# Kernel tuning notes

Measured on AMD Instinct MI355X. Metric: run time of the kernel, lower is better.

## Reference

```python
import jax, jax.numpy as jnp
import numpy as np

N_NODES = 20000
N_EDGES = 640000
IN_DIM, HID_DIM, OUT_DIM = 128, 128, 64


def setup_inputs() -> dict:
    key = jax.random.key(0)
    k = jax.random.split(key, 6)
    x = jax.random.normal(k[0], (N_NODES, IN_DIM), dtype=jnp.float32)
    edge_index = jax.random.randint(k[1], (2, N_EDGES), 0, N_NODES, dtype=jnp.int64)
    W1 = jax.random.normal(k[2], (IN_DIM, HID_DIM), dtype=jnp.float32) * (1.0 / np.sqrt(IN_DIM))
    b1 = jnp.zeros((HID_DIM,), dtype=jnp.float32)
    W2 = jax.random.normal(k[3], (HID_DIM, OUT_DIM), dtype=jnp.float32) * (1.0 / np.sqrt(HID_DIM))
    b2 = jnp.zeros((OUT_DIM,), dtype=jnp.float32)
    return {"x": x, "edge_index": edge_index, "W1": W1, "b1": b1, "W2": W2, "b2": b2}


def _gcn_conv(h, W, b, src, dst, n_nodes):
    # h' = D^-1/2 (A + I) D^-1/2 (h W) + b   (PyG GCNConv with self-loops)
    h = h @ W                                              # [N, F_out]
    ones = jnp.ones((src.shape[0],), dtype=h.dtype)
    deg = jax.ops.segment_sum(ones, dst, num_segments=n_nodes) + 1.0  # +1 for self-loop
    dinv = jax.lax.rsqrt(deg)                              # [N]
    w = dinv[src] * dinv[dst]                              # per-edge norm [E]
    msg = h[src] * w[:, None]                              # gather + scale [E, F_out]
    agg = jax.ops.segment_sum(msg, dst, num_segments=n_nodes)  # scatter-add [N, F_out]
    # self-loop contribution: norm_ii = dinv[i]^2
    return agg + h * (dinv * dinv)[:, None] + b


def reference(x, edge_index, W1, b1, W2, b2):
    src, dst = edge_index[0], edge_index[1]
    n = x.shape[0]
    h = _gcn_conv(x, W1, b1, src, dst, n)
    h = jax.nn.relu(h)
    # dropout is identity in eval mode (training=False)
    out = _gcn_conv(h, W2, b2, src, dst, n)
    return out
```

## Files before the change

### kernel.cpp

```cpp
#include <hip/hip_runtime.h>


#define N_NODES 20000
#define N_EDGES 640000
#define IN_DIM 128
#define HID_DIM 128
#define OUT_DIM 64

#define STRIDE 80
#define SCAT_NB (N_EDGES / 256)
#define G1_NB 625
#define G1_TASKS (2 * (N_NODES / 16))
#define PRE_ITEMS (128 * 128 + 64 * 128 + N_NODES)
#define PRE_NB ((PRE_ITEMS + 255) / 256)

typedef _Float16 half8_t __attribute__((ext_vector_type(8)));
typedef float float4_t __attribute__((ext_vector_type(4)));

__global__ __launch_bounds__(256) void k_pre(const float* __restrict__ W1,
                                             const float* __restrict__ W2,
                                             _Float16* __restrict__ WT1,
                                             _Float16* __restrict__ WT2,
                                             int* __restrict__ cnt) {
    int i = blockIdx.x * 256 + threadIdx.x;
    if (i < 128 * 128) {
        int c = i >> 7, k = i & 127;
        WT1[i] = (_Float16)W1[k * 128 + c];
    } else if (i < 128 * 128 + 64 * 128) {
        int o = i - 128 * 128;
        int c = o >> 7, k = o & 127;
        WT2[o] = (_Float16)W2[k * 64 + c];
    } else {
        int n = i - (128 * 128 + 64 * 128);
        if (n < N_NODES) cnt[n] = 0;
    }
}

__global__ __launch_bounds__(256) void k_front(const int* __restrict__ src,
                                               const int* __restrict__ dst,
                                               int* __restrict__ cnt,
                                               unsigned short* __restrict__ esrc_pad,
                                               const _Float16* __restrict__ WT1,
                                               const float* __restrict__ x,
                                               _Float16* __restrict__ G) {
    const int b = blockIdx.x, tid = threadIdx.x;
    if (b < SCAT_NB) {
        const int e = b * 256 + tid;
        const int s = __builtin_nontemporal_load(&src[e]);
        const int d = __builtin_nontemporal_load(&dst[e]);
        unsigned int rank = atomicAdd((unsigned int*)&cnt[d], 1u);
        if (rank < STRIDE) esrc_pad[d * STRIDE + rank] = (unsigned short)s;
        return;
    }
    const int wave = tid >> 6;
    const int lane = tid & 63;
    const int task = (b - SCAT_NB) * 4 + wave;
    if (task >= G1_TASKS) return;
    const int strip = task >> 1;
    const int nh = task & 1;
    const int row0 = strip * 16;
    const int mrow = row0 + (lane & 15);
    const int kq = (lane >> 4) * 8;

    half8_t af[4];
#pragma unroll
    for (int kc = 0; kc < 4; ++kc) {
        const float* ap = x + (size_t)mrow * 128 + kc * 32 + kq;
        float4_t f0 = __builtin_nontemporal_load((const float4_t*)ap);
        float4_t f1 = __builtin_nontemporal_load((const float4_t*)(ap + 4));
        half8_t h;
        h[0] = (_Float16)f0[0]; h[1] = (_Float16)f0[1];
        h[2] = (_Float16)f0[2]; h[3] = (_Float16)f0[3];
        h[4] = (_Float16)f1[0]; h[5] = (_Float16)f1[1];
        h[6] = (_Float16)f1[2]; h[7] = (_Float16)f1[3];
        af[kc] = h;
    }
    float4_t acc[4];
#pragma unroll
    for (int nt = 0; nt < 4; ++nt) acc[nt] = (float4_t)(0.0f);
#pragma unroll
    for (int nt = 0; nt < 4; ++nt) {
        const _Float16* wp = WT1 + (size_t)((nh * 4 + nt) * 16 + (lane & 15)) * 128 + kq;
#pragma unroll
        for (int kc = 0; kc < 4; ++kc) {
            half8_t bf = *(const half8_t*)(wp + kc * 32);
            acc[nt] = __builtin_amdgcn_mfma_f32_16x16x32_f16(af[kc], bf, acc[nt], 0, 0, 0);
        }
    }
#pragma unroll
    for (int r = 0; r < 4; ++r) {
        int row = row0 + (lane >> 4) * 4 + r;
#pragma unroll
        for (int nt = 0; nt < 4; ++nt)
            G[(size_t)row * 128 + nh * 64 + nt * 16 + (lane & 15)] =
                (_Float16)acc[nt][r];
    }
}

__global__ __launch_bounds__(256) void k_mid(const int* __restrict__ cnt,
                                             const unsigned short* __restrict__ esrc_pad,
                                             const _Float16* __restrict__ G,
                                             const _Float16* __restrict__ WT2,
                                             const float* __restrict__ b1,
                                             _Float16* __restrict__ g2) {
    __shared__ _Float16 h1[16][136];
    const int tid = threadIdx.x;
    const int wave = tid >> 6;
    const int lane = tid & 63;
    const int row0 = blockIdx.x * 16;
    const int eidx = lane >> 4;
    const int fl = lane & 15;

    for (int r4 = 0; r4 < 4; ++r4) {
        const int rr = wave * 4 + r4;
        const int node = row0 + rr;
        const int end = cnt[node];
        const float dvd = rsqrtf((float)end + 1.0f);
        const int base = node * STRIDE;

        float acc[8];
#pragma unroll
        for (int p = 0; p < 8; ++p) acc[p] = 0.0f;
        if (eidx == 0) {
            half8_t sv = *(const half8_t*)(G + (size_t)node * 128 + fl * 8);
#pragma unroll
            for (int p = 0; p < 8; ++p) acc[p] = dvd * (float)sv[p];
        }
        int j = 0;
        for (; j + 7 < end; j += 8) {
            int s0 = (int)__builtin_nontemporal_load(&esrc_pad[base + j + eidx]);
            int s1 = (int)__builtin_nontemporal_load(&esrc_pad[base + j + 4 + eidx]);
            float dv0 = rsqrtf((float)cnt[s0] + 1.0f);
            float dv1 = rsqrtf((float)cnt[s1] + 1.0f);
            half8_t r0 = *(const half8_t*)(G + (size_t)s0 * 128 + fl * 8);
            half8_t r1 = *(const half8_t*)(G + (size_t)s1 * 128 + fl * 8);
#pragma unroll
            for (int p = 0; p < 8; ++p)
                acc[p] += dv0 * (float)r0[p] + dv1 * (float)r1[p];
        }
        for (; j + 3 < end; j += 4) {
            int s = (int)__builtin_nontemporal_load(&esrc_pad[base + j + eidx]);
            float dvs = rsqrtf((float)cnt[s] + 1.0f);
            half8_t r = *(const half8_t*)(G + (size_t)s * 128 + fl * 8);
#pragma unroll
            for (int p = 0; p < 8; ++p) acc[p] += dvs * (float)r[p];
        }
        if (j < end) {
            int idx = j + eidx;
            int s = (int)__builtin_nontemporal_load(
                &esrc_pad[base + ((idx < end) ? idx : (end - 1))]);
            float valid = (idx < end) ? 1.0f : 0.0f;
            float dvs = rsqrtf((float)cnt[s] + 1.0f);
            half8_t r = *(const half8_t*)(G + (size_t)s * 128 + fl * 8);
#pragma unroll
            for (int p = 0; p < 8; ++p) acc[p] += valid * dvs * (float)r[p];
        }
#pragma unroll
        for (int p = 0; p < 8; ++p) {
            acc[p] += __shfl_xor(acc[p], 16, 64);
            acc[p] += __shfl_xor(acc[p], 32, 64);
        }
        if (eidx == 0) {
            float4_t c0 = *(const float4_t*)(b1 + fl * 8);
            float4_t c1 = *(const float4_t*)(b1 + fl * 8 + 4);
            half8_t o;
            o[0] = (_Float16)fmaxf(acc[0] * dvd + c0[0], 0.0f);
            o[1] = (_Float16)fmaxf(acc[1] * dvd + c0[1], 0.0f);
            o[2] = (_Float16)fmaxf(acc[2] * dvd + c0[2], 0.0f);
            o[3] = (_Float16)fmaxf(acc[3] * dvd + c0[3], 0.0f);
            o[4] = (_Float16)fmaxf(acc[4] * dvd + c1[0], 0.0f);
            o[5] = (_Float16)fmaxf(acc[5] * dvd + c1[1], 0.0f);
            o[6] = (_Float16)fmaxf(acc[6] * dvd + c1[2], 0.0f);
            o[7] = (_Float16)fmaxf(acc[7] * dvd + c1[3], 0.0f);
            *(half8_t*)&h1[rr][fl * 8] = o;
        }
    }
    __syncthreads();

    const int fr = lane & 15;
    const int kq = (lane >> 4) * 8;
    half8_t af[4];
#pragma unroll
    for (int kc = 0; kc < 4; ++kc)
        af[kc] = *(const half8_t*)&h1[fr][kc * 32 + kq];
    float4_t acc2 = (float4_t)(0.0f);
    const _Float16* wp = WT2 + (size_t)(wave * 16 + fr) * 128 + kq;
#pragma unroll
    for (int kc = 0; kc < 4; ++kc) {
        half8_t bf = *(const half8_t*)(wp + kc * 32);
        acc2 = __builtin_amdgcn_mfma_f32_16x16x32_f16(af[kc], bf, acc2, 0, 0, 0);
    }
#pragma unroll
    for (int r = 0; r < 4; ++r) {
        int row = row0 + (lane >> 4) * 4 + r;
        g2[(size_t)row * 64 + wave * 16 + fr] = (_Float16)acc2[r];
    }
}

__global__ __launch_bounds__(256) void k_back(const int* __restrict__ cnt,
                                              const unsigned short* __restrict__ esrc_pad,
                                              const _Float16* __restrict__ g2,
                                              const float* __restrict__ b2,
                                              float* __restrict__ out) {
    const int wave = threadIdx.x >> 6;
    const int lane = threadIdx.x & 63;
    const int node = blockIdx.x * 4 + wave;
    if (node >= N_NODES) return;
    const int eidx = lane >> 3;
    const int fl = lane & 7;

    const int end = cnt[node];
    const float dvd = rsqrtf((float)end + 1.0f);
    const int base = node * STRIDE;

    float acc[8];
#pragma unroll
    for (int p = 0; p < 8; ++p) acc[p] = 0.0f;
    if (lane < 8) {
        half8_t s = *(const half8_t*)(g2 + (size_t)node * 64 + fl * 8);
#pragma unroll
        for (int p = 0; p < 8; ++p) acc[p] = dvd * (float)s[p];
    }

    int j = 0;
    for (; j + 15 < end; j += 16) {
        int s0 = (int)__builtin_nontemporal_load(&esrc_pad[base + j + eidx]);
        int s1 = (int)__builtin_nontemporal_load(&esrc_pad[base + j + 8 + eidx]);
        float dv0 = rsqrtf((float)cnt[s0] + 1.0f);
        float dv1 = rsqrtf((float)cnt[s1] + 1.0f);
        half8_t r0 = *(const half8_t*)(g2 + (size_t)s0 * 64 + fl * 8);
        half8_t r1 = *(const half8_t*)(g2 + (size_t)s1 * 64 + fl * 8);
#pragma unroll
        for (int p = 0; p < 8; ++p)
            acc[p] += dv0 * (float)r0[p] + dv1 * (float)r1[p];
    }
    for (; j + 7 < end; j += 8) {
        int s = (int)__builtin_nontemporal_load(&esrc_pad[base + j + eidx]);
        float dvs = rsqrtf((float)cnt[s] + 1.0f);
        half8_t r = *(const half8_t*)(g2 + (size_t)s * 64 + fl * 8);
#pragma unroll
        for (int p = 0; p < 8; ++p) acc[p] += dvs * (float)r[p];
    }
    if (j < end) {
        int idx = j + eidx;
        int s = (int)__builtin_nontemporal_load(
            &esrc_pad[base + ((idx < end) ? idx : (end - 1))]);
        float valid = (idx < end) ? 1.0f : 0.0f;
        float dvs = rsqrtf((float)cnt[s] + 1.0f);
        half8_t r = *(const half8_t*)(g2 + (size_t)s * 64 + fl * 8);
#pragma unroll
        for (int p = 0; p < 8; ++p) acc[p] += valid * dvs * (float)r[p];
    }

#pragma unroll
    for (int p = 0; p < 8; ++p) {
        acc[p] += __shfl_xor(acc[p], 32, 64);
        acc[p] += __shfl_xor(acc[p], 16, 64);
        acc[p] += __shfl_xor(acc[p], 8, 64);
    }

    if (lane < 8) {
        float4_t c0 = *(const float4_t*)(b2 + fl * 8);
        float4_t c1 = *(const float4_t*)(b2 + fl * 8 + 4);
        float4_t o0, o1;
        o0[0] = acc[0] * dvd + c0[0]; o0[1] = acc[1] * dvd + c0[1];
        o0[2] = acc[2] * dvd + c0[2]; o0[3] = acc[3] * dvd + c0[3];
        o1[0] = acc[4] * dvd + c1[0]; o1[1] = acc[5] * dvd + c1[1];
        o1[2] = acc[6] * dvd + c1[2]; o1[3] = acc[7] * dvd + c1[3];
        __builtin_nontemporal_store(o0, (float4_t*)(out + (size_t)node * 64 + fl * 8));
        __builtin_nontemporal_store(o1, (float4_t*)(out + (size_t)node * 64 + fl * 8 + 4));
    }
}

extern "C" void kernel_launch(void* const* d_in, const int* in_sizes, int n_in,
                              void* d_out, int out_size, void* d_ws, size_t ws_size,
                              hipStream_t stream) {
    const float* x  = (const float*)d_in[0];
    const int*   ei = (const int*)d_in[1];
    const float* W1 = (const float*)d_in[2];
    const float* b1 = (const float*)d_in[3];
    const float* W2 = (const float*)d_in[4];
    const float* b2 = (const float*)d_in[5];

    const int* src = ei;
    const int* dst = ei + N_EDGES;

    char* w = (char*)d_ws;
    unsigned short* esrc_pad = (unsigned short*)w; w += sizeof(unsigned short) * (size_t)N_NODES * STRIDE;
    _Float16*       G        = (_Float16*)w;       w += sizeof(_Float16) * (size_t)N_NODES * 128;
    _Float16*       g2       = (_Float16*)w;       w += sizeof(_Float16) * (size_t)N_NODES * OUT_DIM;
    _Float16*       WT1      = (_Float16*)w;       w += sizeof(_Float16) * 128 * 128;
    _Float16*       WT2      = (_Float16*)w;       w += sizeof(_Float16) * 64 * 128;
    int*            cnt      = (int*)w;            w += sizeof(int) * N_NODES;
    float*          out      = (float*)d_out;

    k_pre<<<PRE_NB, 256, 0, stream>>>(W1, W2, WT1, WT2, cnt);
    k_front<<<SCAT_NB + G1_NB, 256, 0, stream>>>(src, dst, cnt, esrc_pad, WT1, x, G);
    k_mid<<<N_NODES / 16, 256, 0, stream>>>(cnt, esrc_pad, G, WT2, b1, g2);
    k_back<<<(N_NODES + 3) / 4, 256, 0, stream>>>(cnt, esrc_pad, g2, b2, out);
}
```

Measured before the change: 165.9 us.

## Split hidden features into halves, range-partition edge scatter, prescale layer-2 features

Edge bucketing is reorganized so each block scans a chunk of edges but only inserts those whose destination lies in one of eight node ranges, which localizes atomics and writes at the cost of reading dst eight times. The hidden feature matrix is stored as two 64-wide halves, and the layer-1 aggregation processes each half with 8 lanes per row and 8 edges in parallel, for better cache footprint per gather. The layer-2 source-degree normalization is folded into g2 when it is written, removing per-edge cnt lookups and rsqrt in the final gather. Neighbor counts are also clamped to STRIDE when reading.

```diff
diff --git a/kernel.cpp b/kernel.cpp
--- a/kernel.cpp
+++ b/kernel.cpp
@@ -8,7 +8,11 @@
 #define OUT_DIM 64
 
 #define STRIDE 80
-#define SCAT_NB (N_EDGES / 256)
+#define NRANGE 8
+#define RANGE_SZ (N_NODES / NRANGE)
+#define SCAT_NB 2048
+#define CHUNKS (SCAT_NB / NRANGE)
+#define EPC (N_EDGES / CHUNKS)
 #define G1_NB 625
 #define G1_TASKS (2 * (N_NODES / 16))
 #define PRE_ITEMS (128 * 128 + 64 * 128 + N_NODES)
@@ -42,14 +46,22 @@
                                                unsigned short* __restrict__ esrc_pad,
                                                const _Float16* __restrict__ WT1,
                                                const float* __restrict__ x,
-                                               _Float16* __restrict__ G) {
+                                               _Float16* __restrict__ GA,
+                                               _Float16* __restrict__ GB) {
     const int b = blockIdx.x, tid = threadIdx.x;
     if (b < SCAT_NB) {
-        const int e = b * 256 + tid;
-        const int s = __builtin_nontemporal_load(&src[e]);
-        const int d = __builtin_nontemporal_load(&dst[e]);
-        unsigned int rank = atomicAdd((unsigned int*)&cnt[d], 1u);
-        if (rank < STRIDE) esrc_pad[d * STRIDE + rank] = (unsigned short)s;
+        const int g = b & 7;
+        const int lo = g * RANGE_SZ;
+        const int e0 = (b >> 3) * EPC;
+        for (int i = tid; i < EPC; i += 256) {
+            const int e = e0 + i;
+            const int d = __builtin_nontemporal_load(&dst[e]);
+            if ((unsigned int)(d - lo) < (unsigned int)RANGE_SZ) {
+                const int s = __builtin_nontemporal_load(&src[e]);
+                unsigned int rank = atomicAdd((unsigned int*)&cnt[d], 1u);
+                if (rank < STRIDE) esrc_pad[d * STRIDE + rank] = (unsigned short)s;
+            }
+        }
         return;
     }
     const int wave = tid >> 6;
@@ -61,6 +73,7 @@
     const int row0 = strip * 16;
     const int mrow = row0 + (lane & 15);
     const int kq = (lane >> 4) * 8;
+    _Float16* G = nh ? GB : GA;
 
     half8_t af[4];
 #pragma unroll
@@ -92,14 +105,14 @@
         int row = row0 + (lane >> 4) * 4 + r;
 #pragma unroll
         for (int nt = 0; nt < 4; ++nt)
-            G[(size_t)row * 128 + nh * 64 + nt * 16 + (lane & 15)] =
-                (_Float16)acc[nt][r];
+            G[(size_t)row * 64 + nt * 16 + (lane & 15)] = (_Float16)acc[nt][r];
     }
 }
 
 __global__ __launch_bounds__(256) void k_mid(const int* __restrict__ cnt,
                                              const unsigned short* __restrict__ esrc_pad,
-                                             const _Float16* __restrict__ G,
+                                             const _Float16* __restrict__ GA,
+                                             const _Float16* __restrict__ GB,
                                              const _Float16* __restrict__ WT2,
                                              const float* __restrict__ b1,
                                              _Float16* __restrict__ g2) {
@@ -108,71 +121,76 @@
     const int wave = tid >> 6;
     const int lane = tid & 63;
     const int row0 = blockIdx.x * 16;
-    const int eidx = lane >> 4;
-    const int fl = lane & 15;
-
-    for (int r4 = 0; r4 < 4; ++r4) {
-        const int rr = wave * 4 + r4;
-        const int node = row0 + rr;
-        const int end = cnt[node];
-        const float dvd = rsqrtf((float)end + 1.0f);
-        const int base = node * STRIDE;
-
-        float acc[8];
-#pragma unroll
-        for (int p = 0; p < 8; ++p) acc[p] = 0.0f;
-        if (eidx == 0) {
-            half8_t sv = *(const half8_t*)(G + (size_t)node * 128 + fl * 8);
-#pragma unroll
-            for (int p = 0; p < 8; ++p) acc[p] = dvd * (float)sv[p];
-        }
-        int j = 0;
-        for (; j + 7 < end; j += 8) {
-            int s0 = (int)__builtin_nontemporal_load(&esrc_pad[base + j + eidx]);
-            int s1 = (int)__builtin_nontemporal_load(&esrc_pad[base + j + 4 + eidx]);
-            float dv0 = rsqrtf((float)cnt[s0] + 1.0f);
-            float dv1 = rsqrtf((float)cnt[s1] + 1.0f);
-            half8_t r0 = *(const half8_t*)(G + (size_t)s0 * 128 + fl * 8);
-            half8_t r1 = *(const half8_t*)(G + (size_t)s1 * 128 + fl * 8);
-#pragma unroll
-            for (int p = 0; p < 8; ++p)
-                acc[p] += dv0 * (float)r0[p] + dv1 * (float)r1[p];
-        }
-        for (; j + 3 < end; j += 4) {
-            int s = (int)__builtin_nontemporal_load(&esrc_pad[base + j + eidx]);
-            float dvs = rsqrtf((float)cnt[s] + 1.0f);
-            half8_t r = *(const half8_t*)(G + (size_t)s * 128 + fl * 8);
-#pragma unroll
-            for (int p = 0; p < 8; ++p) acc[p] += dvs * (float)r[p];
-        }
-        if (j < end) {
-            int idx = j + eidx;
-            int s = (int)__builtin_nontemporal_load(
-                &esrc_pad[base + ((idx < end) ? idx : (end - 1))]);
-            float valid = (idx < end) ? 1.0f : 0.0f;
-            float dvs = rsqrtf((float)cnt[s] + 1.0f);
-            half8_t r = *(const half8_t*)(G + (size_t)s * 128 + fl * 8);
-#pragma unroll
-            for (int p = 0; p < 8; ++p) acc[p] += valid * dvs * (float)r[p];
-        }
-#pragma unroll
-        for (int p = 0; p < 8; ++p) {
-            acc[p] += __shfl_xor(acc[p], 16, 64);
-            acc[p] += __shfl_xor(acc[p], 32, 64);
-        }
-        if (eidx == 0) {
-            float4_t c0 = *(const float4_t*)(b1 + fl * 8);
-            float4_t c1 = *(const float4_t*)(b1 + fl * 8 + 4);
-            half8_t o;
-            o[0] = (_Float16)fmaxf(acc[0] * dvd + c0[0], 0.0f);
-            o[1] = (_Float16)fmaxf(acc[1] * dvd + c0[1], 0.0f);
-            o[2] = (_Float16)fmaxf(acc[2] * dvd + c0[2], 0.0f);
-            o[3] = (_Float16)fmaxf(acc[3] * dvd + c0[3], 0.0f);
-            o[4] = (_Float16)fmaxf(acc[4] * dvd + c1[0], 0.0f);
-            o[5] = (_Float16)fmaxf(acc[5] * dvd + c1[1], 0.0f);
-            o[6] = (_Float16)fmaxf(acc[6] * dvd + c1[2], 0.0f);
-            o[7] = (_Float16)fmaxf(acc[7] * dvd + c1[3], 0.0f);
-            *(half8_t*)&h1[rr][fl * 8] = o;
+    const int eidx = lane >> 3;
+    const int fl = lane & 7;
+
+    for (int h = 0; h < 2; ++h) {
+        const _Float16* __restrict__ G = h ? GB : GA;
+        for (int r4 = 0; r4 < 4; ++r4) {
+            const int rr = wave * 4 + r4;
+            const int node = row0 + rr;
+            const int endt = cnt[node];
+            const float dvd = rsqrtf((float)endt + 1.0f);
+            const int end = endt < STRIDE ? endt : STRIDE;
+            const int base = node * STRIDE;
+
+            float acc[8];
+#pragma unroll
+            for (int p = 0; p < 8; ++p) acc[p] = 0.0f;
+            if (lane < 8) {
+                half8_t sv = *(const half8_t*)(G + (size_t)node * 64 + fl * 8);
+#pragma unroll
+                for (int p = 0; p < 8; ++p) acc[p] = dvd * (float)sv[p];
+            }
+            int j = 0;
+            for (; j + 15 < end; j += 16) {
+                int s0 = (int)__builtin_nontemporal_load(&esrc_pad[base + j + eidx]);
+                int s1 = (int)__builtin_nontemporal_load(&esrc_pad[base + j + 8 + eidx]);
+                float dv0 = rsqrtf((float)cnt[s0] + 1.0f);
+                float dv1 = rsqrtf((float)cnt[s1] + 1.0f);
+                half8_t r0 = *(const half8_t*)(G + (size_t)s0 * 64 + fl * 8);
+                half8_t r1 = *(const half8_t*)(G + (size_t)s1 * 64 + fl * 8);
+#pragma unroll
+                for (int p = 0; p < 8; ++p)
+                    acc[p] += dv0 * (float)r0[p] + dv1 * (float)r1[p];
+            }
+            for (; j + 7 < end; j += 8) {
+                int s = (int)__builtin_nontemporal_load(&esrc_pad[base + j + eidx]);
+                float dvs = rsqrtf((float)cnt[s] + 1.0f);
+                half8_t r = *(const half8_t*)(G + (size_t)s * 64 + fl * 8);
+#pragma unroll
+                for (int p = 0; p < 8; ++p) acc[p] += dvs * (float)r[p];
+            }
+            if (j < end) {
+                int idx = j + eidx;
+                int s = (int)__builtin_nontemporal_load(
+                    &esrc_pad[base + ((idx < end) ? idx : (end - 1))]);
+                float valid = (idx < end) ? 1.0f : 0.0f;
+                float dvs = rsqrtf((float)cnt[s] + 1.0f);
+                half8_t r = *(const half8_t*)(G + (size_t)s * 64 + fl * 8);
+#pragma unroll
+                for (int p = 0; p < 8; ++p) acc[p] += valid * dvs * (float)r[p];
+            }
+#pragma unroll
+            for (int p = 0; p < 8; ++p) {
+                acc[p] += __shfl_xor(acc[p], 32, 64);
+                acc[p] += __shfl_xor(acc[p], 16, 64);
+                acc[p] += __shfl_xor(acc[p], 8, 64);
+            }
+            if (lane < 8) {
+                float4_t c0 = *(const float4_t*)(b1 + h * 64 + fl * 8);
+                float4_t c1 = *(const float4_t*)(b1 + h * 64 + fl * 8 + 4);
+                half8_t o;
+                o[0] = (_Float16)fmaxf(acc[0] * dvd + c0[0], 0.0f);
+                o[1] = (_Float16)fmaxf(acc[1] * dvd + c0[1], 0.0f);
+                o[2] = (_Float16)fmaxf(acc[2] * dvd + c0[2], 0.0f);
+                o[3] = (_Float16)fmaxf(acc[3] * dvd + c0[3], 0.0f);
+                o[4] = (_Float16)fmaxf(acc[4] * dvd + c1[0], 0.0f);
+                o[5] = (_Float16)fmaxf(acc[5] * dvd + c1[1], 0.0f);
+                o[6] = (_Float16)fmaxf(acc[6] * dvd + c1[2], 0.0f);
+                o[7] = (_Float16)fmaxf(acc[7] * dvd + c1[3], 0.0f);
+                *(half8_t*)&h1[rr][h * 64 + fl * 8] = o;
+            }
         }
     }
     __syncthreads();
@@ -193,7 +211,8 @@
 #pragma unroll
     for (int r = 0; r < 4; ++r) {
         int row = row0 + (lane >> 4) * 4 + r;
-        g2[(size_t)row * 64 + wave * 16 + fr] = (_Float16)acc2[r];
+        float dvr = rsqrtf((float)cnt[row] + 1.0f);
+        g2[(size_t)row * 64 + wave * 16 + fr] = (_Float16)(dvr * acc2[r]);
     }
 }
 
@@ -209,8 +228,9 @@
     const int eidx = lane >> 3;
     const int fl = lane & 7;
 
-    const int end = cnt[node];
-    const float dvd = rsqrtf((float)end + 1.0f);
+    const int endt = cnt[node];
+    const float dvd = rsqrtf((float)endt + 1.0f);
+    const int end = endt < STRIDE ? endt : STRIDE;
     const int base = node * STRIDE;
 
     float acc[8];
@@ -219,37 +239,32 @@
     if (lane < 8) {
         half8_t s = *(const half8_t*)(g2 + (size_t)node * 64 + fl * 8);
 #pragma unroll
-        for (int p = 0; p < 8; ++p) acc[p] = dvd * (float)s[p];
+        for (int p = 0; p < 8; ++p) acc[p] = (float)s[p];
     }
 
     int j = 0;
     for (; j + 15 < end; j += 16) {
         int s0 = (int)__builtin_nontemporal_load(&esrc_pad[base + j + eidx]);
         int s1 = (int)__builtin_nontemporal_load(&esrc_pad[base + j + 8 + eidx]);
-        float dv0 = rsqrtf((float)cnt[s0] + 1.0f);
-        float dv1 = rsqrtf((float)cnt[s1] + 1.0f);
         half8_t r0 = *(const half8_t*)(g2 + (size_t)s0 * 64 + fl * 8);
         half8_t r1 = *(const half8_t*)(g2 + (size_t)s1 * 64 + fl * 8);
 #pragma unroll
-        for (int p = 0; p < 8; ++p)
-            acc[p] += dv0 * (float)r0[p] + dv1 * (float)r1[p];
+        for (int p = 0; p < 8; ++p) acc[p] += (float)r0[p] + (float)r1[p];
     }
     for (; j + 7 < end; j += 8) {
         int s = (int)__builtin_nontemporal_load(&esrc_pad[base + j + eidx]);
-        float dvs = rsqrtf((float)cnt[s] + 1.0f);
         half8_t r = *(const half8_t*)(g2 + (size_t)s * 64 + fl * 8);
 #pragma unroll
-        for (int p = 0; p < 8; ++p) acc[p] += dvs * (float)r[p];
+        for (int p = 0; p < 8; ++p) acc[p] += (float)r[p];
     }
     if (j < end) {
         int idx = j + eidx;
         int s = (int)__builtin_nontemporal_load(
             &esrc_pad[base + ((idx < end) ? idx : (end - 1))]);
         float valid = (idx < end) ? 1.0f : 0.0f;
-        float dvs = rsqrtf((float)cnt[s] + 1.0f);
         half8_t r = *(const half8_t*)(g2 + (size_t)s * 64 + fl * 8);
 #pragma unroll
-        for (int p = 0; p < 8; ++p) acc[p] += valid * dvs * (float)r[p];
+        for (int p = 0; p < 8; ++p) acc[p] += valid * (float)r[p];
     }
 
 #pragma unroll
@@ -287,7 +302,8 @@
 
     char* w = (char*)d_ws;
     unsigned short* esrc_pad = (unsigned short*)w; w += sizeof(unsigned short) * (size_t)N_NODES * STRIDE;
-    _Float16*       G        = (_Float16*)w;       w += sizeof(_Float16) * (size_t)N_NODES * 128;
+    _Float16*       GA       = (_Float16*)w;       w += sizeof(_Float16) * (size_t)N_NODES * 64;
+    _Float16*       GB       = (_Float16*)w;       w += sizeof(_Float16) * (size_t)N_NODES * 64;
     _Float16*       g2       = (_Float16*)w;       w += sizeof(_Float16) * (size_t)N_NODES * OUT_DIM;
     _Float16*       WT1      = (_Float16*)w;       w += sizeof(_Float16) * 128 * 128;
     _Float16*       WT2      = (_Float16*)w;       w += sizeof(_Float16) * 64 * 128;
@@ -295,7 +311,7 @@
     float*          out      = (float*)d_out;
 
     k_pre<<<PRE_NB, 256, 0, stream>>>(W1, W2, WT1, WT2, cnt);
-    k_front<<<SCAT_NB + G1_NB, 256, 0, stream>>>(src, dst, cnt, esrc_pad, WT1, x, G);
-    k_mid<<<N_NODES / 16, 256, 0, stream>>>(cnt, esrc_pad, G, WT2, b1, g2);
+    k_front<<<SCAT_NB + G1_NB, 256, 0, stream>>>(src, dst, cnt, esrc_pad, WT1, x, GA, GB);
+    k_mid<<<N_NODES / 16, 256, 0, stream>>>(cnt, esrc_pad, GA, GB, WT2, b1, g2);
     k_back<<<(N_NODES + 3) / 4, 256, 0, stream>>>(cnt, esrc_pad, g2, b2, out);
 }
```

Result: slower. 178.6 us (+7.7%).
